# Kernel tuning notes

Hardware: AMD Instinct MI355X
Metric: run time of the kernel (lower is better)

Reference implementation:

```python
import jax, jax.numpy as jnp
import numpy as np

D_MODEL = 1024
N_HEAD = 16


def setup_inputs() -> dict:
    key = jax.random.key(0)
    ks = jax.random.split(key, 13)
    B, S, D = 2, 2048, D_MODEL
    scale = 1.0 / np.sqrt(D)
    inp = {
        "q": jax.random.normal(ks[0], (B, S, D), jnp.float32),
        "k": jax.random.normal(ks[1], (B, S, D), jnp.float32),
        "v": jax.random.normal(ks[2], (B, S, D), jnp.float32),
        "mask": jax.random.randint(ks[3], (1, 1, S, S), 0, 2, jnp.int32),
        "Wq": jax.random.normal(ks[4], (D, D), jnp.float32) * scale,
        "bq": jnp.zeros((D,), jnp.float32),
        "Wk": jax.random.normal(ks[5], (D, D), jnp.float32) * scale,
        "bk": jnp.zeros((D,), jnp.float32),
        "Wv": jax.random.normal(ks[6], (D, D), jnp.float32) * scale,
        "bv": jnp.zeros((D,), jnp.float32),
        "Wo": jax.random.normal(ks[7], (D, D), jnp.float32) * scale,
        "bo": jnp.zeros((D,), jnp.float32),
    }
    return inp


def _split_heads(x, n_head):
    # [B, S, D] -> [B, H, S, Dh]
    B, S, D = x.shape
    return x.reshape(B, S, n_head, D // n_head).transpose(0, 2, 1, 3)


def reference(q, k, v, mask, Wq, bq, Wk, bk, Wv, bv, Wo, bo):
    # linear projections (torch Linear: x @ W.T + b)
    qp = q @ Wq.T + bq
    kp = k @ Wk.T + bk
    vp = v @ Wv.T + bv
    qh = _split_heads(qp, N_HEAD)  # [B,H,S,Dh]
    kh = _split_heads(kp, N_HEAD)
    vh = _split_heads(vp, N_HEAD)
    d_k = qh.shape[-1]
    scores = jnp.einsum("bhqd,bhkd->bhqk", qh, kh) / jnp.sqrt(jnp.asarray(d_k, qh.dtype))
    neg = jnp.finfo(qh.dtype).min
    scores = jnp.where(mask == 0, neg, scores)
    attn = jax.nn.softmax(scores, axis=-1)
    out = jnp.einsum("bhqk,bhkd->bhqd", attn, vh)  # [B,H,S,Dh]
    B, H, S, Dh = out.shape
    concat = out.transpose(0, 2, 1, 3).reshape(B, S, H * Dh)
    return concat @ Wo.T + bo
```

## Files before the change

kernel.cpp:

```cpp
#include <hip/hip_runtime.h>
#include <hip/hip_bf16.h>

typedef __attribute__((ext_vector_type(8))) short short8;
typedef __attribute__((ext_vector_type(4))) float f32x4;
typedef __attribute__((ext_vector_type(4))) float floatv4;
typedef __attribute__((ext_vector_type(4))) unsigned int u32x4;
typedef unsigned short u16;
typedef unsigned int u32;
typedef unsigned long long u64;

#define S_LEN 2048
#define DMODEL 1024
#define NHEAD 16
#define DHEAD 64

__device__ __forceinline__ u16 f2bf(float f) {
  __hip_bfloat16 h = __float2bfloat16(f);
  return __builtin_bit_cast(u16, h);
}

__device__ __forceinline__ u32 cvtpk(float lo, float hi) {
  u32 r;
  asm("v_cvt_pk_bf16_f32 %0, %1, %2" : "=v"(r) : "v"(lo), "v"(hi));
  return r;
}

__device__ __forceinline__ void gload16(const void* g, void* l) {
  __builtin_amdgcn_global_load_lds(
      (const __attribute__((address_space(1))) u32*)g,
      (__attribute__((address_space(3))) u32*)l, 16, 0, 0);
}

__device__ __forceinline__ f32x4 mfma16(short8 a, short8 b, f32x4 c) {
  return __builtin_amdgcn_mfma_f32_16x16x32_bf16(a, b, c, 0, 0, 0);
}

__global__ void k_convert_qkv(const float* __restrict__ q, const float* __restrict__ k,
                              const float* __restrict__ v, u16* __restrict__ qb,
                              u16* __restrict__ kb, u16* __restrict__ vb) {
  const float* src = blockIdx.y == 0 ? q : blockIdx.y == 1 ? k : v;
  u16* dst = blockIdx.y == 0 ? qb : blockIdx.y == 1 ? kb : vb;
  int i = blockIdx.x * blockDim.x + threadIdx.x;
  floatv4 w = reinterpret_cast<const floatv4*>(src)[i];
  ushort4 o;
  o.x = f2bf(w.x); o.y = f2bf(w.y); o.z = f2bf(w.z); o.w = f2bf(w.w);
  reinterpret_cast<ushort4*>(dst)[i] = o;
}

__global__ void k_convert_w(const float* __restrict__ w0, const float* __restrict__ w1,
                            const float* __restrict__ w2, const float* __restrict__ w3,
                            u16* __restrict__ d0, u16* __restrict__ d1,
                            u16* __restrict__ d2, u16* __restrict__ d3) {
  const int z = blockIdx.y;
  const float* src = z == 0 ? w0 : z == 1 ? w1 : z == 2 ? w2 : w3;
  u16* dst = z == 0 ? d0 : z == 1 ? d1 : z == 2 ? d2 : d3;
  int i = blockIdx.x * blockDim.x + threadIdx.x;
  floatv4 w = reinterpret_cast<const floatv4*>(src)[i];
  ushort4 o;
  o.x = f2bf(w.x); o.y = f2bf(w.y); o.z = f2bf(w.z); o.w = f2bf(w.w);
  reinterpret_cast<ushort4*>(dst)[i] = o;
}

__global__ void k_maskpack(const int* __restrict__ mask, u64* __restrict__ bits) {
  int tid = blockIdx.x * blockDim.x + threadIdx.x;
  u64 b = __ballot(mask[tid] != 0);
  if ((threadIdx.x & 63) == 0) bits[tid >> 6] = b;
}

template <int BN>
__device__ __forceinline__ void gemm_body(const u16* __restrict__ A,
                                          const u16* __restrict__ W,
                                          const float* __restrict__ bias,
                                          void* __restrict__ dst, int mode,
                                          float scale) {
  constexpr int BM = 128, BK = 32, K = DMODEL;
  constexpr int MI = (BN == 128) ? 4 : 2;
  __shared__ u16 As[2][BM * BK];
  __shared__ u16 Bs[2][BN * BK];
  const int t = threadIdx.x;
  const int lane = t & 63, w = t >> 6;
  const int lr = lane & 15, lg = lane >> 4;
  const int wrow = (BN == 128) ? (w >> 1) * 64 : w * 32;
  const int wcol = (BN == 128) ? (w & 1) * 64 : 0;
  const int brow = blockIdx.y * BM, bcol = blockIdx.x * BN;

  const int sr = t >> 2, scg = (t & 3) * 8;
  const u16* Abase = A + (size_t)(brow + sr) * K + scg;
  const u16* Wbase = W + (size_t)(bcol + sr) * K + scg;

  f32x4 acc[MI][4] = {};

  auto stage = [&](int buf, int kt) {
    const int k0 = kt * BK;
    gload16(Abase + k0, &As[buf][w * 512]);
    gload16(Abase + (size_t)64 * K + k0, &As[buf][2048 + w * 512]);
    gload16(Wbase + k0, &Bs[buf][w * 512]);
    if constexpr (BN == 128)
      gload16(Wbase + (size_t)64 * K + k0, &Bs[buf][2048 + w * 512]);
  };

  stage(0, 0);
  __syncthreads();

  int cur = 0;
  constexpr int NT = K / BK;
  for (int kt = 0; kt < NT; ++kt) {
    if (kt + 1 < NT) stage(cur ^ 1, kt + 1);
    short8 af[MI], bfr[4];
#pragma unroll
    for (int i = 0; i < MI; ++i)
      af[i] = *(const short8*)&As[cur][(wrow + i * 16 + lr) * BK + lg * 8];
#pragma unroll
    for (int j = 0; j < 4; ++j)
      bfr[j] = *(const short8*)&Bs[cur][(wcol + j * 16 + lr) * BK + lg * 8];
#pragma unroll
    for (int i = 0; i < MI; ++i)
#pragma unroll
      for (int j = 0; j < 4; ++j)
        acc[i][j] = mfma16(af[i], bfr[j], acc[i][j]);
    __syncthreads();
    cur ^= 1;
  }

#pragma unroll
  for (int i = 0; i < MI; ++i) {
#pragma unroll
    for (int j = 0; j < 4; ++j) {
#pragma unroll
      for (int r = 0; r < 4; ++r) {
        const int m = brow + wrow + i * 16 + lg * 4 + r;
        const int n = bcol + wcol + j * 16 + lr;
        const float v = (acc[i][j][r] + bias[n]) * scale;
        if (mode == 0) {
          const int b = m >> 11, s = m & (S_LEN - 1), h = n >> 6, dh = n & 63;
          ((u16*)dst)[((size_t)(b * NHEAD + h) * S_LEN + s) * DHEAD + dh] = f2bf(v);
        } else if (mode == 1) {
          const int b = m >> 11, s = m & (S_LEN - 1), h = n >> 6, dh = n & 63;
          ((u16*)dst)[((size_t)(b * NHEAD + h) * DHEAD + dh) * S_LEN + s] = f2bf(v);
        } else {
          ((float*)dst)[(size_t)m * DMODEL + n] = v;
        }
      }
    }
  }
}

__global__ __launch_bounds__(256, 2) void k_gemm_qkv(
    const u16* __restrict__ qb, const u16* __restrict__ kb, const u16* __restrict__ vb,
    const u16* __restrict__ Wqb, const u16* __restrict__ Wkb, const u16* __restrict__ Wvb,
    const float* __restrict__ bq, const float* __restrict__ bk, const float* __restrict__ bv,
    u16* __restrict__ qh, u16* __restrict__ kh, u16* __restrict__ vT) {
  const int z = blockIdx.z;
  const u16* A = z == 0 ? qb : z == 1 ? kb : vb;
  const u16* W = z == 0 ? Wqb : z == 1 ? Wkb : Wvb;
  const float* b = z == 0 ? bq : z == 1 ? bk : bv;
  void* dst = z == 0 ? (void*)qh : z == 1 ? (void*)kh : (void*)vT;
  const float scale = z == 0 ? 0.125f * 1.44269504f : 1.0f;
  gemm_body<128>(A, W, b, dst, z == 2 ? 1 : 0, scale);
}

__global__ __launch_bounds__(256, 2) void k_gemm_out(
    const u16* __restrict__ A, const u16* __restrict__ W,
    const float* __restrict__ bias, float* __restrict__ dst) {
  gemm_body<64>(A, W, bias, dst, 2, 1.0f);
}

__global__ __launch_bounds__(256, 4) void k_attn(
    const u16* __restrict__ Qh, const u16* __restrict__ Kh,
    const u16* __restrict__ Vt, const u64* __restrict__ Mb,
    u16* __restrict__ O) {
  constexpr int KB = 64;
  constexpr int NT = S_LEN / KB;
  constexpr int VP = 72;
  __shared__ u16 Ks[2][KB * DHEAD];
  __shared__ u16 Vs[2][DHEAD * VP];
  const int t = threadIdx.x, lane = t & 63, w = t >> 6;
  const int lr = lane & 15, lg = lane >> 4;
  const int qt = blockIdx.x, bh = blockIdx.y;
  const size_t base = (size_t)bh * S_LEN * DHEAD;
  const int q0 = qt * 64;
  const int qrow = q0 + w * 16 + lr;

  short8 qf[2];
  {
    const u16* qp = Qh + base + (size_t)qrow * DHEAD + lg * 8;
    qf[0] = *(const short8*)qp;
    qf[1] = *(const short8*)(qp + 32);
  }

  f32x4 oacc[4] = {};
  float mrun = -1e30f, lrun = 0.f;

  const int sr = t >> 3;
  const int scg_k = (((t & 7) ^ (sr & 7)) * 8);
  const int c8 = (t & 7) * 8;

  auto stageK = [&](int buf, int kt2) {
    const int kb0 = kt2 * KB;
    gload16(Kh + base + (size_t)(kb0 + sr) * DHEAD + scg_k, &Ks[buf][w * 512]);
    gload16(Kh + base + (size_t)(kb0 + 32 + sr) * DHEAD + scg_k, &Ks[buf][2048 + w * 512]);
  };
  const u16* vsrc0 = Vt + base + (size_t)sr * S_LEN + c8;
  const u16* vsrc1 = Vt + base + (size_t)(sr + 32) * S_LEN + c8;

  short8 va = *(const short8*)(vsrc0);
  short8 vbr = *(const short8*)(vsrc1);
  stageK(0, 0);
  *(short8*)&Vs[0][sr * VP + c8] = va;
  *(short8*)&Vs[0][(sr + 32) * VP + c8] = vbr;
  __syncthreads();

  u64 mw_next = Mb[(size_t)qrow * (S_LEN / 64)];

  const int rsw = lr & 7;
  const int kc0 = (lg ^ rsw) * 8, kc1 = ((lg + 4) ^ rsw) * 8;

  int cur = 0;
  for (int kt2 = 0; kt2 < NT; ++kt2) {
    const u64 mw = mw_next;
    if (kt2 + 1 < NT) {
      mw_next = Mb[(size_t)qrow * (S_LEN / 64) + kt2 + 1];
      const int kb1 = (kt2 + 1) * KB;
      va = *(const short8*)(vsrc0 + kb1);
      vbr = *(const short8*)(vsrc1 + kb1);
      stageK(cur ^ 1, kt2 + 1);
    }

    f32x4 sc[4];
#pragma unroll
    for (int j = 0; j < 4; ++j) {
      f32x4 c = {};
      short8 k0 = *(const short8*)&Ks[cur][(j * 16 + lr) * 64 + kc0];
      short8 k1 = *(const short8*)&Ks[cur][(j * 16 + lr) * 64 + kc1];
      c = mfma16(k0, qf[0], c);
      c = mfma16(k1, qf[1], c);
      sc[j] = c;
    }

    const u32 mlo = (u32)(mw >> (lg * 4));
    const u32 mhi = (u32)(mw >> (32 + lg * 4));
#pragma unroll
    for (int j = 0; j < 4; ++j) {
      const u32 msrc = (j < 2) ? mlo : mhi;
      const int sh = (j & 1) * 16;
#pragma unroll
      for (int r = 0; r < 4; ++r)
        sc[j][r] = ((msrc >> (sh + r)) & 1u) ? sc[j][r] : -1e30f;
    }

    float pm;
    {
      float a0 = fmaxf(sc[0][0], sc[0][1]), a1 = fmaxf(sc[0][2], sc[0][3]);
      float a2 = fmaxf(sc[1][0], sc[1][1]), a3 = fmaxf(sc[1][2], sc[1][3]);
      float a4 = fmaxf(sc[2][0], sc[2][1]), a5 = fmaxf(sc[2][2], sc[2][3]);
      float a6 = fmaxf(sc[3][0], sc[3][1]), a7 = fmaxf(sc[3][2], sc[3][3]);
      float b0 = fmaxf(a0, a1), b1 = fmaxf(a2, a3), b2 = fmaxf(a4, a5), b3 = fmaxf(a6, a7);
      pm = fmaxf(fmaxf(b0, b1), fmaxf(b2, b3));
    }
    pm = fmaxf(pm, __shfl_xor(pm, 16));
    pm = fmaxf(pm, __shfl_xor(pm, 32));

    if (!__all(pm <= mrun + 8.0f)) {
      float mnew = fmaxf(mrun, pm);
      float alpha = exp2f(mrun - mnew);
      lrun *= alpha;
      mrun = mnew;
      float aC[4];
#pragma unroll
      for (int r = 0; r < 4; ++r) aC[r] = __shfl(alpha, lg * 4 + r);
#pragma unroll
      for (int jo = 0; jo < 4; ++jo)
#pragma unroll
        for (int r = 0; r < 4; ++r) oacc[jo][r] *= aC[r];
    }

#pragma unroll
    for (int j = 0; j < 4; ++j)
#pragma unroll
      for (int r = 0; r < 4; ++r) sc[j][r] = exp2f(sc[j][r] - mrun);
    float ps;
    {
      float a0 = sc[0][0] + sc[0][1], a1 = sc[0][2] + sc[0][3];
      float a2 = sc[1][0] + sc[1][1], a3 = sc[1][2] + sc[1][3];
      float a4 = sc[2][0] + sc[2][1], a5 = sc[2][2] + sc[2][3];
      float a6 = sc[3][0] + sc[3][1], a7 = sc[3][2] + sc[3][3];
      ps = ((a0 + a1) + (a2 + a3)) + ((a4 + a5) + (a6 + a7));
    }
    ps += __shfl_xor(ps, 16);
    ps += __shfl_xor(ps, 32);
    lrun += ps;

    u32x4 pa1 = {cvtpk(sc[0][0], sc[0][1]), cvtpk(sc[0][2], sc[0][3]),
                 cvtpk(sc[1][0], sc[1][1]), cvtpk(sc[1][2], sc[1][3])};
    u32x4 pa2 = {cvtpk(sc[2][0], sc[2][1]), cvtpk(sc[2][2], sc[2][3]),
                 cvtpk(sc[3][0], sc[3][1]), cvtpk(sc[3][2], sc[3][3])};
    short8 A1 = __builtin_bit_cast(short8, pa1);
    short8 A2 = __builtin_bit_cast(short8, pa2);

#pragma unroll
    for (int jo = 0; jo < 4; ++jo) {
      const u16* Vrow = &Vs[cur][(jo * 16 + lr) * VP + lg * 4];
      union { ushort4 h[2]; short8 s8; } vb1, vb2;
      vb1.h[0] = *(const ushort4*)&Vrow[0];
      vb1.h[1] = *(const ushort4*)&Vrow[16];
      vb2.h[0] = *(const ushort4*)&Vrow[32];
      vb2.h[1] = *(const ushort4*)&Vrow[48];
      oacc[jo] = mfma16(A1, vb1.s8, oacc[jo]);
      oacc[jo] = mfma16(A2, vb2.s8, oacc[jo]);
    }

    if (kt2 + 1 < NT) {
      *(short8*)&Vs[cur ^ 1][sr * VP + c8] = va;
      *(short8*)&Vs[cur ^ 1][(sr + 32) * VP + c8] = vbr;
    }
    __syncthreads();
    cur ^= 1;
  }

  const int b = bh >> 4, h = bh & 15;
  const float invq = 1.0f / lrun;
  float inv[4];
#pragma unroll
  for (int r = 0; r < 4; ++r) inv[r] = __shfl(invq, lg * 4 + r);
#pragma unroll
  for (int jo = 0; jo < 4; ++jo)
#pragma unroll
    for (int r = 0; r < 4; ++r) {
      const int s = q0 + w * 16 + lg * 4 + r;
      const float o = oacc[jo][r] * inv[r];
      O[((size_t)(b * S_LEN + s)) * DMODEL + h * DHEAD + jo * 16 + lr] = f2bf(o);
    }
}

extern "C" void kernel_launch(void* const* d_in, const int* in_sizes, int n_in,
                              void* d_out, int out_size, void* d_ws, size_t ws_size,
                              hipStream_t stream) {
  const float* q = (const float*)d_in[0];
  const float* k = (const float*)d_in[1];
  const float* v = (const float*)d_in[2];
  const int* mask = (const int*)d_in[3];
  const float* Wq = (const float*)d_in[4];
  const float* bq = (const float*)d_in[5];
  const float* Wk = (const float*)d_in[6];
  const float* bk = (const float*)d_in[7];
  const float* Wv = (const float*)d_in[8];
  const float* bv = (const float*)d_in[9];
  const float* Wo = (const float*)d_in[10];
  const float* bo = (const float*)d_in[11];

  char* ws = (char*)d_ws;
  const size_t MB = 1024 * 1024;
  u16* qb  = (u16*)(ws + 0 * MB);
  u16* kb  = (u16*)(ws + 8 * MB);
  u16* vb  = (u16*)(ws + 16 * MB);
  u16* Wqb = (u16*)(ws + 24 * MB);
  u16* Wkb = (u16*)(ws + 26 * MB);
  u16* Wvb = (u16*)(ws + 28 * MB);
  u16* Wob = (u16*)(ws + 30 * MB);
  u16* qh  = (u16*)(ws + 32 * MB);
  u16* kh  = (u16*)(ws + 40 * MB);
  u16* vT  = (u16*)(ws + 48 * MB);
  u16* cc  = (u16*)(ws + 56 * MB);
  u64* mb  = (u64*)(ws + 64 * MB);

  k_convert_qkv<<<dim3(4096, 3), 256, 0, stream>>>(q, k, v, qb, kb, vb);
  k_convert_w<<<dim3(1024, 4), 256, 0, stream>>>(Wq, Wk, Wv, Wo, Wqb, Wkb, Wvb, Wob);
  k_maskpack<<<16384, 256, 0, stream>>>(mask, mb);

  k_gemm_qkv<<<dim3(8, 32, 3), 256, 0, stream>>>(qb, kb, vb, Wqb, Wkb, Wvb,
                                                 bq, bk, bv, qh, kh, vT);

  k_attn<<<dim3(S_LEN / 64, 32), 256, 0, stream>>>(qh, kh, vT, mb, cc);

  k_gemm_out<<<dim3(16, 32), 256, 0, stream>>>(cc, Wob, bo, (float*)d_out);
}
```

Baseline: 178.3 us.

## Fuse fp32-to-bf16 activation conversion into QKV projection GEMM loader

Removes the separate q/k/v conversion kernel and has the QKV GEMM read fp32 activations directly. Each tile's values are converted to bf16 in registers with packed cvt instructions and written to LDS after the MFMAs, overlapping the global loads with compute. This avoids writing and re-reading 24MB of bf16 intermediates and one kernel launch. In exchange the A-tile path uses register-staged loads instead of direct global-to-LDS loads and reads twice as many bytes per tile, and the occupancy hint rises from 2 to 3 blocks.

```diff
diff --git a/kernel.cpp b/kernel.cpp
--- a/kernel.cpp
+++ b/kernel.cpp
@@ -33,18 +33,6 @@
 
 __device__ __forceinline__ f32x4 mfma16(short8 a, short8 b, f32x4 c) {
   return __builtin_amdgcn_mfma_f32_16x16x32_bf16(a, b, c, 0, 0, 0);
-}
-
-__global__ void k_convert_qkv(const float* __restrict__ q, const float* __restrict__ k,
-                              const float* __restrict__ v, u16* __restrict__ qb,
-                              u16* __restrict__ kb, u16* __restrict__ vb) {
-  const float* src = blockIdx.y == 0 ? q : blockIdx.y == 1 ? k : v;
-  u16* dst = blockIdx.y == 0 ? qb : blockIdx.y == 1 ? kb : vb;
-  int i = blockIdx.x * blockDim.x + threadIdx.x;
-  floatv4 w = reinterpret_cast<const floatv4*>(src)[i];
-  ushort4 o;
-  o.x = f2bf(w.x); o.y = f2bf(w.y); o.z = f2bf(w.z); o.w = f2bf(w.w);
-  reinterpret_cast<ushort4*>(dst)[i] = o;
 }
 
 __global__ void k_convert_w(const float* __restrict__ w0, const float* __restrict__ w1,
@@ -57,7 +45,7 @@
   int i = blockIdx.x * blockDim.x + threadIdx.x;
   floatv4 w = reinterpret_cast<const floatv4*>(src)[i];
   ushort4 o;
-  o.x = f2bf(w.x); o.y = f2bf(w.y); o.z = f2bf(w.z); o.w = f2bf(w.w);
+  o.x = f2bf(w[0]); o.y = f2bf(w[1]); o.z = f2bf(w[2]); o.w = f2bf(w[3]);
   reinterpret_cast<ushort4*>(dst)[i] = o;
 }
 
@@ -67,8 +55,8 @@
   if ((threadIdx.x & 63) == 0) bits[tid >> 6] = b;
 }
 
-template <int BN>
-__device__ __forceinline__ void gemm_body(const u16* __restrict__ A,
+template <int BN, bool AFP32>
+__device__ __forceinline__ void gemm_body(const void* __restrict__ Av,
                                           const u16* __restrict__ W,
                                           const float* __restrict__ bias,
                                           void* __restrict__ dst, int mode,
@@ -85,27 +73,61 @@
   const int brow = blockIdx.y * BM, bcol = blockIdx.x * BN;
 
   const int sr = t >> 2, scg = (t & 3) * 8;
-  const u16* Abase = A + (size_t)(brow + sr) * K + scg;
   const u16* Wbase = W + (size_t)(bcol + sr) * K + scg;
+  const u16* Ab = nullptr;
+  const float* Af0 = nullptr;
+  if constexpr (AFP32) {
+    Af0 = (const float*)Av + (size_t)(brow + sr) * K + scg;
+  } else {
+    Ab = (const u16*)Av + (size_t)(brow + sr) * K + scg;
+  }
 
   f32x4 acc[MI][4] = {};
 
-  auto stage = [&](int buf, int kt) {
+  auto stageW = [&](int buf, int kt) {
     const int k0 = kt * BK;
-    gload16(Abase + k0, &As[buf][w * 512]);
-    gload16(Abase + (size_t)64 * K + k0, &As[buf][2048 + w * 512]);
     gload16(Wbase + k0, &Bs[buf][w * 512]);
     if constexpr (BN == 128)
       gload16(Wbase + (size_t)64 * K + k0, &Bs[buf][2048 + w * 512]);
   };
 
-  stage(0, 0);
+  if constexpr (AFP32) {
+    floatv4 a0 = *(const floatv4*)(Af0);
+    floatv4 a1 = *(const floatv4*)(Af0 + 4);
+    floatv4 a2 = *(const floatv4*)(Af0 + (size_t)64 * K);
+    floatv4 a3 = *(const floatv4*)(Af0 + (size_t)64 * K + 4);
+    stageW(0, 0);
+    u32x4 p0 = {cvtpk(a0[0], a0[1]), cvtpk(a0[2], a0[3]),
+                cvtpk(a1[0], a1[1]), cvtpk(a1[2], a1[3])};
+    u32x4 p1 = {cvtpk(a2[0], a2[1]), cvtpk(a2[2], a2[3]),
+                cvtpk(a3[0], a3[1]), cvtpk(a3[2], a3[3])};
+    *(short8*)&As[0][sr * BK + scg] = __builtin_bit_cast(short8, p0);
+    *(short8*)&As[0][(sr + 64) * BK + scg] = __builtin_bit_cast(short8, p1);
+  } else {
+    gload16(Ab, &As[0][w * 512]);
+    gload16(Ab + (size_t)64 * K, &As[0][2048 + w * 512]);
+    stageW(0, 0);
+  }
   __syncthreads();
 
   int cur = 0;
   constexpr int NT = K / BK;
   for (int kt = 0; kt < NT; ++kt) {
-    if (kt + 1 < NT) stage(cur ^ 1, kt + 1);
+    floatv4 a0, a1, a2, a3;
+    if (kt + 1 < NT) {
+      const int k1 = (kt + 1) * BK;
+      if constexpr (AFP32) {
+        a0 = *(const floatv4*)(Af0 + k1);
+        a1 = *(const floatv4*)(Af0 + k1 + 4);
+        a2 = *(const floatv4*)(Af0 + (size_t)64 * K + k1);
+        a3 = *(const floatv4*)(Af0 + (size_t)64 * K + k1 + 4);
+      } else {
+        gload16(Ab + k1, &As[cur ^ 1][w * 512]);
+        gload16(Ab + (size_t)64 * K + k1, &As[cur ^ 1][2048 + w * 512]);
+      }
+      stageW(cur ^ 1, kt + 1);
+    }
+
     short8 af[MI], bfr[4];
 #pragma unroll
     for (int i = 0; i < MI; ++i)
@@ -118,6 +140,17 @@
 #pragma unroll
       for (int j = 0; j < 4; ++j)
         acc[i][j] = mfma16(af[i], bfr[j], acc[i][j]);
+
+    if constexpr (AFP32) {
+      if (kt + 1 < NT) {
+        u32x4 p0 = {cvtpk(a0[0], a0[1]), cvtpk(a0[2], a0[3]),
+                    cvtpk(a1[0], a1[1]), cvtpk(a1[2], a1[3])};
+        u32x4 p1 = {cvtpk(a2[0], a2[1]), cvtpk(a2[2], a2[3]),
+                    cvtpk(a3[0], a3[1]), cvtpk(a3[2], a3[3])};
+        *(short8*)&As[cur ^ 1][sr * BK + scg] = __builtin_bit_cast(short8, p0);
+        *(short8*)&As[cur ^ 1][(sr + 64) * BK + scg] = __builtin_bit_cast(short8, p1);
+      }
+    }
     __syncthreads();
     cur ^= 1;
   }
@@ -145,24 +178,24 @@
   }
 }
 
-__global__ __launch_bounds__(256, 2) void k_gemm_qkv(
-    const u16* __restrict__ qb, const u16* __restrict__ kb, const u16* __restrict__ vb,
+__global__ __launch_bounds__(256, 3) void k_gemm_qkv(
+    const float* __restrict__ q, const float* __restrict__ k, const float* __restrict__ v,
     const u16* __restrict__ Wqb, const u16* __restrict__ Wkb, const u16* __restrict__ Wvb,
     const float* __restrict__ bq, const float* __restrict__ bk, const float* __restrict__ bv,
     u16* __restrict__ qh, u16* __restrict__ kh, u16* __restrict__ vT) {
   const int z = blockIdx.z;
-  const u16* A = z == 0 ? qb : z == 1 ? kb : vb;
+  const float* A = z == 0 ? q : z == 1 ? k : v;
   const u16* W = z == 0 ? Wqb : z == 1 ? Wkb : Wvb;
   const float* b = z == 0 ? bq : z == 1 ? bk : bv;
   void* dst = z == 0 ? (void*)qh : z == 1 ? (void*)kh : (void*)vT;
   const float scale = z == 0 ? 0.125f * 1.44269504f : 1.0f;
-  gemm_body<128>(A, W, b, dst, z == 2 ? 1 : 0, scale);
+  gemm_body<128, true>(A, W, b, dst, z == 2 ? 1 : 0, scale);
 }
 
 __global__ __launch_bounds__(256, 2) void k_gemm_out(
     const u16* __restrict__ A, const u16* __restrict__ W,
     const float* __restrict__ bias, float* __restrict__ dst) {
-  gemm_body<64>(A, W, bias, dst, 2, 1.0f);
+  gemm_body<64, false>(A, W, bias, dst, 2, 1.0f);
 }
 
 __global__ __launch_bounds__(256, 4) void k_attn(
@@ -350,9 +383,6 @@
 
   char* ws = (char*)d_ws;
   const size_t MB = 1024 * 1024;
-  u16* qb  = (u16*)(ws + 0 * MB);
-  u16* kb  = (u16*)(ws + 8 * MB);
-  u16* vb  = (u16*)(ws + 16 * MB);
   u16* Wqb = (u16*)(ws + 24 * MB);
   u16* Wkb = (u16*)(ws + 26 * MB);
   u16* Wvb = (u16*)(ws + 28 * MB);
@@ -363,11 +393,10 @@
   u16* cc  = (u16*)(ws + 56 * MB);
   u64* mb  = (u64*)(ws + 64 * MB);
 
-  k_convert_qkv<<<dim3(4096, 3), 256, 0, stream>>>(q, k, v, qb, kb, vb);
   k_convert_w<<<dim3(1024, 4), 256, 0, stream>>>(Wq, Wk, Wv, Wo, Wqb, Wkb, Wvb, Wob);
   k_maskpack<<<16384, 256, 0, stream>>>(mask, mb);
 
-  k_gemm_qkv<<<dim3(8, 32, 3), 256, 0, stream>>>(qb, kb, vb, Wqb, Wkb, Wvb,
+  k_gemm_qkv<<<dim3(8, 32, 3), 256, 0, stream>>>(q, k, v, Wqb, Wkb, Wvb,
                                                  bq, bk, bv, qh, kh, vT);
 
   k_attn<<<dim3(S_LEN / 64, 32), 256, 0, stream>>>(qh, kh, vT, mb, cc);
```

After: 190.5 us. 6.8% more time.
